# Optimization experiments

Measured on AMD Instinct MI355X. Metric: run time of the kernel, lower is better.

The kernel has to match this reference:

```python
import jax, jax.numpy as jnp
import numpy as np

K = 3  # kernel_size
P = K * K  # patch length per channel


def setup_inputs() -> dict:
    key = jax.random.key(0)
    k1, k2 = jax.random.split(key)
    B, H, W, C_in, C_out = 16, 64, 64, 64, 64
    L = P * (P + 1) // 2 + P + 1  # 45 quadratic + 9 linear + 1 bias = 55
    x = jax.random.normal(k1, (B, H, W, C_in), dtype=jnp.float32)
    # glorot-ish scale for the flat kernel [1,1,L,C_in,C_out]
    flat_kernel = jax.random.normal(k2, (1, 1, L, C_in, C_out), dtype=jnp.float32) * 0.05
    return {"x": x, "flat_kernel": flat_kernel}


def _quadratic_features(x):
    # x: [B,H,W,C] NHWC; stride 1, 'same' padding, k=3
    B, H, W, C = x.shape
    pad = K // 2
    xp = jnp.pad(x, ((0, 0), (pad, pad), (pad, pad), (0, 0)))
    # patches: [B,H,W,P,C] -- loop is over the 9 fixed kernel taps only
    patches = jnp.stack(
        [xp[:, i:i + H, j:j + W, :] for i in range(K) for j in range(K)], axis=3
    )
    iu, ju = np.triu_indices(P)  # all pairs i<=j incl. squares -> 45 terms
    quad = patches[:, :, :, iu, :] * patches[:, :, :, ju, :]  # [B,H,W,45,C]
    ones = jnp.ones_like(patches[:, :, :, :1, :])              # bias term
    # flat features per the use_linear_and_bias=True layout: [quad | linear | 1]
    return jnp.concatenate([quad, patches, ones], axis=3)       # [B,H,W,55,C]


def reference(x, flat_kernel):
    feats = _quadratic_features(x)          # [B,H,W,L,C]
    w = flat_kernel[0, 0]                   # [L,C,O]
    # contract over flat-feature index L and input channels C
    return jnp.einsum('bhwlc,lco->bhwo', feats, w)
```

## Files before the change

kernel.cpp:

```cpp
#include <hip/hip_runtime.h>

typedef _Float16 half8 __attribute__((ext_vector_type(8)));
typedef _Float16 half4v __attribute__((ext_vector_type(4)));
typedef float f32x16 __attribute__((ext_vector_type(16)));

#define RING_OFF 33792
#define LDS_TOTAL (33792 + 16384)

__device__ __forceinline__ void stage4(const void* g, void* l) {
  __builtin_amdgcn_global_load_lds(
      (const __attribute__((address_space(1))) unsigned int*)(unsigned long long)g,
      (__attribute__((address_space(3))) unsigned int*)(unsigned int)(unsigned long long)l,
      4, 0, 0);
}

__global__ __launch_bounds__(256)
void prepack_kernel(const float* __restrict__ W, _Float16* __restrict__ Bp) {
  const int idx = blockIdx.x * 256 + threadIdx.x;
  if (idx < 221184) {
    const int v   = idx & 7;
    const int lam = (idx >> 3) & 63;
    const int f   = idx >> 9;
    const int nt  = f & 1;
    const int ks  = (f >> 1) & 1;
    const int lf  = (f >> 2) % 54;
    const int cp  = (f >> 2) / 54;
    const int cc  = ks * 2 + cp;
    const int c   = cc * 16 + (lam >> 5) * 8 + v;
    const int o   = nt * 32 + (lam & 31);
    Bp[idx] = (_Float16)W[(lf * 64 + c) * 64 + o];
  } else if (idx < 221184 + 64) {
    const int o = idx - 221184;
    float s = 0.f;
    for (int c = 0; c < 64; ++c) s += W[(54 * 64 + c) * 64 + o];
    ((float*)(Bp + 221184))[o] = s;
  }
}

__global__ __launch_bounds__(1024, 4)
void qconv_kernel(const float* __restrict__ x, const _Float16* __restrict__ Bp,
                  float* __restrict__ out) {
  constexpr int IU[45] = {0,0,0,0,0,0,0,0,0, 1,1,1,1,1,1,1,1, 2,2,2,2,2,2,2,
                          3,3,3,3,3,3, 4,4,4,4,4, 5,5,5,5, 6,6,6, 7,7, 8};
  constexpr int JU[45] = {0,1,2,3,4,5,6,7,8, 1,2,3,4,5,6,7,8, 2,3,4,5,6,7,8,
                          3,4,5,6,7,8, 4,5,6,7,8, 5,6,7,8, 6,7,8, 7,8, 8};

  const int tid  = threadIdx.x;
  const int wave = tid >> 6;
  const int lane = tid & 63;
  const int mh   = wave & 3;
  const int nt   = (wave >> 2) & 1;
  const int ks   = wave >> 3;
  const int b    = blockIdx.x >> 5;
  const int h0   = (blockIdx.x & 31) * 2;

  __shared__ __align__(16) unsigned char smem[LDS_TOTAL];

  for (int idx = tid; idx < 4 * 66 * 16; idx += 1024) {
    const int row = idx / (66 * 16);
    const int rem = idx - row * (66 * 16);
    const int col = rem >> 4;
    const int cg  = rem & 15;
    const int hs  = h0 - 1 + row;
    const int w   = col - 1;
    float4 v = make_float4(0.f, 0.f, 0.f, 0.f);
    if ((unsigned)hs < 64u && (unsigned)w < 64u)
      v = *(const float4*)(x + ((((size_t)b * 64 + hs) * 64 + w) * 64 + cg * 4));
    half4v hv;
    hv[0] = (_Float16)v.x; hv[1] = (_Float16)v.y;
    hv[2] = (_Float16)v.z; hv[3] = (_Float16)v.w;
    const int addr = (row * 8448 + col * 128 + cg * 8) ^ ((col & 7) << 4);
    *(half4v*)(smem + addr) = hv;
  }
  __syncthreads();

  const char* BpB = (const char*)Bp;
  const int wbase = wave * 256;

#define STAGE(SPG) do {                                                  \
    const char* s_ = BpB + (SPG) * 8192 + tid * 4;                       \
    char* d_ = (char*)smem + RING_OFF + ((SPG) & 1) * 8192 + wbase;      \
    stage4(s_, d_); stage4(s_ + 4096, d_ + 4096);                        \
  } while (0)

  STAGE(0); STAGE(1);

  f32x16 acc = {};
  const int colA = lane & 31;
  const int kg   = lane >> 5;
  const int r0   = mh >> 1;
  const int wseg = mh & 1;
  const unsigned fbase = RING_OFF + (ks * 2 + nt) * 1024 + lane * 16;

#pragma unroll
  for (int cp = 0; cp < 2; ++cp) {
    const int cc    = ks * 2 + cp;
    const int cbyte = cc * 32 + kg * 16;

    half8 tap[9];
#pragma unroll
    for (int t = 0; t < 9; ++t) {
      const int ce = wseg * 32 + colA + (t % 3);
      const int a  = ((r0 + t / 3) * 8448 + ce * 128 + cbyte) ^ ((ce & 7) << 4);
      tap[t] = *(const half8*)(smem + a);
    }

#pragma unroll
    for (int s = 0; s < 27; ++s) {
      const int spg = cp * 27 + s;
      if (spg < 53) { asm volatile("s_waitcnt vmcnt(2)" ::: "memory"); }
      else          { asm volatile("s_waitcnt vmcnt(0)" ::: "memory"); }
      __builtin_amdgcn_s_barrier();
#pragma unroll
      for (int j = 0; j < 2; ++j) {
        const int l = s * 2 + j;
        const half8 bf =
            *(const half8*)(smem + (spg & 1) * 8192 + j * 4096 + fbase);
        half8 a;
        if (l < 45) a = tap[IU[l]] * tap[JU[l]];
        else        a = tap[l - 45];
        acc = __builtin_amdgcn_mfma_f32_32x32x16_f16(a, bf, acc, 0, 0, 0);
      }
      asm volatile("s_waitcnt lgkmcnt(0)" ::: "memory");
      __builtin_amdgcn_s_barrier();
      if (spg < 52) STAGE(spg + 2);
    }
  }
#undef STAGE

  __syncthreads();
  float* red = (float*)smem;
  const int colD = lane & 31;
  const int rg   = lane >> 5;

  if (ks == 1) {
#pragma unroll
    for (int g = 0; g < 16; ++g) {
      const int rowD = (g & 3) + 8 * (g >> 2) + 4 * rg;
      red[(mh * 2 + nt) * 1024 + rowD * 32 + colD] = acc[g];
    }
  }
  __syncthreads();
  if (ks == 0) {
    const float bias = ((const float*)(Bp + 221184))[nt * 32 + colD];
    float* op = out + (((size_t)b * 64 + h0 + r0) * 64 + wseg * 32) * 64
                    + nt * 32 + colD;
#pragma unroll
    for (int g = 0; g < 16; ++g) {
      const int rowD = (g & 3) + 8 * (g >> 2) + 4 * rg;
      op[(size_t)rowD * 64] =
          acc[g] + red[(mh * 2 + nt) * 1024 + rowD * 32 + colD] + bias;
    }
  }
}

extern "C" void kernel_launch(void* const* d_in, const int* in_sizes, int n_in,
                              void* d_out, int out_size, void* d_ws, size_t ws_size,
                              hipStream_t stream) {
  const float* x = (const float*)d_in[0];
  const float* W = (const float*)d_in[1];
  float* out     = (float*)d_out;
  _Float16* Bp   = (_Float16*)d_ws;

  prepack_kernel<<<dim3((221248 + 255) / 256), dim3(256), 0, stream>>>(W, Bp);
  qconv_kernel<<<dim3(512), dim3(1024), 0, stream>>>(x, Bp, out);
}
```

Before: 49.63 us.

## Shrink block to 4 waves, each computing four M-tiles to reuse B fragments

After: 66.49 us. +34.0%, slower.

```diff
diff --git a/kernel.cpp b/kernel.cpp
--- a/kernel.cpp
+++ b/kernel.cpp
@@ -4,14 +4,15 @@
 typedef _Float16 half4v __attribute__((ext_vector_type(4)));
 typedef float f32x16 __attribute__((ext_vector_type(16)));
 
-#define RING_OFF 33792
-#define LDS_TOTAL (33792 + 16384)
+#define XS 33792
+#define SLOT 12288
+#define LDS_TOTAL (XS + 2 * SLOT)
 
-__device__ __forceinline__ void stage4(const void* g, void* l) {
+__device__ __forceinline__ void stage16(const void* g, const void* l) {
   __builtin_amdgcn_global_load_lds(
       (const __attribute__((address_space(1))) unsigned int*)(unsigned long long)g,
       (__attribute__((address_space(3))) unsigned int*)(unsigned int)(unsigned long long)l,
-      4, 0, 0);
+      16, 0, 0);
 }
 
 __global__ __launch_bounds__(256)
@@ -22,13 +23,12 @@
     const int lam = (idx >> 3) & 63;
     const int f   = idx >> 9;
     const int nt  = f & 1;
-    const int ks  = (f >> 1) & 1;
-    const int lf  = (f >> 2) % 54;
-    const int cp  = (f >> 2) / 54;
-    const int cc  = ks * 2 + cp;
+    const int lr  = f >> 1;
+    const int l   = lr % 54;
+    const int cc  = lr / 54;
     const int c   = cc * 16 + (lam >> 5) * 8 + v;
     const int o   = nt * 32 + (lam & 31);
-    Bp[idx] = (_Float16)W[(lf * 64 + c) * 64 + o];
+    Bp[idx] = (_Float16)W[(l * 64 + c) * 64 + o];
   } else if (idx < 221184 + 64) {
     const int o = idx - 221184;
     float s = 0.f;
@@ -37,7 +37,7 @@
   }
 }
 
-__global__ __launch_bounds__(1024, 4)
+__global__ __launch_bounds__(256, 2)
 void qconv_kernel(const float* __restrict__ x, const _Float16* __restrict__ Bp,
                   float* __restrict__ out) {
   constexpr int IU[45] = {0,0,0,0,0,0,0,0,0, 1,1,1,1,1,1,1,1, 2,2,2,2,2,2,2,
@@ -48,15 +48,27 @@
   const int tid  = threadIdx.x;
   const int wave = tid >> 6;
   const int lane = tid & 63;
-  const int mh   = wave & 3;
-  const int nt   = (wave >> 2) & 1;
-  const int ks   = wave >> 3;
+  const int nt   = wave & 1;
+  const int ks   = wave >> 1;
   const int b    = blockIdx.x >> 5;
   const int h0   = (blockIdx.x & 31) * 2;
 
   __shared__ __align__(16) unsigned char smem[LDS_TOTAL];
+  const char* BpB = (const char*)Bp;
 
-  for (int idx = tid; idx < 4 * 66 * 16; idx += 1024) {
+#pragma unroll
+  for (int q = 0; q < 2; ++q) {
+#pragma unroll
+    for (int g = 0; g < 3; ++g) {
+      const int off = g * 4096 + wave * 1024;
+      const int isB = off >= 6144;
+      const int rel = off - (isB ? 6144 : 0);
+      stage16(BpB + (size_t)((isB * 2) * 54 + q * 3) * 2048 + rel + lane * 16,
+              smem + XS + q * SLOT + off);
+    }
+  }
+
+  for (int idx = tid; idx < 4 * 66 * 16; idx += 256) {
     const int row = idx / (66 * 16);
     const int rem = idx - row * (66 * 16);
     const int col = rem >> 4;
@@ -74,82 +86,94 @@
   }
   __syncthreads();
 
-  const char* BpB = (const char*)Bp;
-  const int wbase = wave * 256;
-
-#define STAGE(SPG) do {                                                  \
-    const char* s_ = BpB + (SPG) * 8192 + tid * 4;                       \
-    char* d_ = (char*)smem + RING_OFF + ((SPG) & 1) * 8192 + wbase;      \
-    stage4(s_, d_); stage4(s_ + 4096, d_ + 4096);                        \
-  } while (0)
-
-  STAGE(0); STAGE(1);
-
-  f32x16 acc = {};
+  f32x16 acc[4] = {};
   const int colA = lane & 31;
   const int kg   = lane >> 5;
-  const int r0   = mh >> 1;
-  const int wseg = mh & 1;
-  const unsigned fbase = RING_OFF + (ks * 2 + nt) * 1024 + lane * 16;
+
+  for (int h = 0; h < 2; ++h) {
+    const int cc    = ks * 2 + h;
+    const int cbyte = cc * 32 + kg * 16;
+
+    half8 tap[4][9];
+#pragma unroll
+    for (int mt = 0; mt < 4; ++mt)
+#pragma unroll
+      for (int t = 0; t < 9; ++t) {
+        const int ce = (mt & 1) * 32 + colA + (t % 3);
+        const int a  = (((mt >> 1) + t / 3) * 8448 + ce * 128 + cbyte)
+                       ^ ((ce & 7) << 4);
+        tap[mt][t] = *(const half8*)(smem + a);
+      }
 
 #pragma unroll
-  for (int cp = 0; cp < 2; ++cp) {
-    const int cc    = ks * 2 + cp;
-    const int cbyte = cc * 32 + kg * 16;
-
-    half8 tap[9];
+    for (int pl = 0; pl < 18; ++pl) {
+      asm volatile("s_waitcnt vmcnt(3)" ::: "memory");
+      __builtin_amdgcn_s_barrier();
+      const unsigned sb = XS + (pl & 1) * SLOT + ks * 6144 + nt * 1024
+                          + lane * 16;
+      const half8 bf0 = *(const half8*)(smem + sb);
+      const half8 bf1 = *(const half8*)(smem + sb + 2048);
+      const half8 bf2 = *(const half8*)(smem + sb + 4096);
+      __builtin_amdgcn_s_setprio(1);
 #pragma unroll
-    for (int t = 0; t < 9; ++t) {
-      const int ce = wseg * 32 + colA + (t % 3);
-      const int a  = ((r0 + t / 3) * 8448 + ce * 128 + cbyte) ^ ((ce & 7) << 4);
-      tap[t] = *(const half8*)(smem + a);
-    }
-
+      for (int j = 0; j < 3; ++j) {
+        const int l = pl * 3 + j;
+        const half8 bf = (j == 0) ? bf0 : ((j == 1) ? bf1 : bf2);
 #pragma unroll
-    for (int s = 0; s < 27; ++s) {
-      const int spg = cp * 27 + s;
-      if (spg < 53) { asm volatile("s_waitcnt vmcnt(2)" ::: "memory"); }
-      else          { asm volatile("s_waitcnt vmcnt(0)" ::: "memory"); }
-      __builtin_amdgcn_s_barrier();
-#pragma unroll
-      for (int j = 0; j < 2; ++j) {
-        const int l = s * 2 + j;
-        const half8 bf =
-            *(const half8*)(smem + (spg & 1) * 8192 + j * 4096 + fbase);
-        half8 a;
-        if (l < 45) a = tap[IU[l]] * tap[JU[l]];
-        else        a = tap[l - 45];
-        acc = __builtin_amdgcn_mfma_f32_32x32x16_f16(a, bf, acc, 0, 0, 0);
+        for (int mt = 0; mt < 4; ++mt) {
+          half8 a;
+          if (l < 45) a = tap[mt][IU[l]] * tap[mt][JU[l]];
+          else        a = tap[mt][l - 45];
+          acc[mt] = __builtin_amdgcn_mfma_f32_32x32x16_f16(a, bf, acc[mt],
+                                                           0, 0, 0);
+        }
       }
+      __builtin_amdgcn_s_setprio(0);
       asm volatile("s_waitcnt lgkmcnt(0)" ::: "memory");
       __builtin_amdgcn_s_barrier();
-      if (spg < 52) STAGE(spg + 2);
+      const int hq  = (pl <= 15) ? h : 1 - h;
+      const int lq0 = ((pl <= 15) ? (pl + 2) : (pl - 16)) * 3;
+#pragma unroll
+      for (int g = 0; g < 3; ++g) {
+        const int off = g * 4096 + wave * 1024;
+        const int isB = off >= 6144;
+        const int rel = off - (isB ? 6144 : 0);
+        stage16(BpB + (size_t)((isB * 2 + hq) * 54 + lq0) * 2048 + rel
+                    + lane * 16,
+                smem + XS + (pl & 1) * SLOT + off);
+      }
     }
   }
-#undef STAGE
 
+  asm volatile("s_waitcnt vmcnt(0)" ::: "memory");
   __syncthreads();
+
   float* red = (float*)smem;
   const int colD = lane & 31;
   const int rg   = lane >> 5;
 
   if (ks == 1) {
 #pragma unroll
-    for (int g = 0; g < 16; ++g) {
-      const int rowD = (g & 3) + 8 * (g >> 2) + 4 * rg;
-      red[(mh * 2 + nt) * 1024 + rowD * 32 + colD] = acc[g];
-    }
+    for (int mt = 0; mt < 4; ++mt)
+#pragma unroll
+      for (int g = 0; g < 16; ++g) {
+        const int rowD = (g & 3) + 8 * (g >> 2) + 4 * rg;
+        red[((nt * 4 + mt) * 32 + rowD) * 32 + colD] = acc[mt][g];
+      }
   }
   __syncthreads();
   if (ks == 0) {
     const float bias = ((const float*)(Bp + 221184))[nt * 32 + colD];
-    float* op = out + (((size_t)b * 64 + h0 + r0) * 64 + wseg * 32) * 64
-                    + nt * 32 + colD;
 #pragma unroll
-    for (int g = 0; g < 16; ++g) {
-      const int rowD = (g & 3) + 8 * (g >> 2) + 4 * rg;
-      op[(size_t)rowD * 64] =
-          acc[g] + red[(mh * 2 + nt) * 1024 + rowD * 32 + colD] + bias;
+    for (int mt = 0; mt < 4; ++mt) {
+      float* op = out + (((size_t)b * 64 + h0 + (mt >> 1)) * 64
+                         + (mt & 1) * 32) * 64 + nt * 32 + colD;
+#pragma unroll
+      for (int g = 0; g < 16; ++g) {
+        const int rowD = (g & 3) + 8 * (g >> 2) + 4 * rg;
+        op[(size_t)rowD * 64] =
+            acc[mt][g] + red[((nt * 4 + mt) * 32 + rowD) * 32 + colD] + bias;
+      }
     }
   }
 }
@@ -163,5 +187,5 @@
   _Float16* Bp   = (_Float16*)d_ws;
 
   prepack_kernel<<<dim3((221248 + 255) / 256), dim3(256), 0, stream>>>(W, Bp);
-  qconv_kernel<<<dim3(512), dim3(1024), 0, stream>>>(x, Bp, out);
+  qconv_kernel<<<dim3(512), dim3(256), 0, stream>>>(x, Bp, out);
 }
```
